# Kernel tuning notes

Hardware: AMD Instinct MI355X
Metric: run time of the kernel (lower is better)

The kernel has to match this reference:

```python
import jax, jax.numpy as jnp
import numpy as np

NEG_SLOPE = 0.2


def _gat_conv(x, edge_index, W, a_src, a_dst, b, heads, out_ch, concat):
    N = x.shape[0]
    # add self loops (PyG GATConv default)
    loops = jnp.arange(N, dtype=edge_index.dtype)
    src = jnp.concatenate([edge_index[0], loops])
    dst = jnp.concatenate([edge_index[1], loops])

    h = (x @ W).reshape(N, heads, out_ch)            # [N,H,C]
    alpha_s = jnp.einsum('nhc,hc->nh', h, a_src)     # [N,H]
    alpha_d = jnp.einsum('nhc,hc->nh', h, a_dst)     # [N,H]
    e = jax.nn.leaky_relu(alpha_s[src] + alpha_d[dst], NEG_SLOPE)  # [E,H]

    # softmax over incoming edges of each dst node (every node has a self loop)
    m = jax.ops.segment_max(e, dst, num_segments=N)  # [N,H]
    e = jnp.exp(e - m[dst])
    denom = jax.ops.segment_sum(e, dst, num_segments=N)  # [N,H]
    alpha = e / denom[dst]                           # [E,H]

    out = jax.ops.segment_sum(h[src] * alpha[..., None], dst, num_segments=N)  # [N,H,C]
    out = out.reshape(N, heads * out_ch) if concat else out.mean(axis=1)
    return out + b


def setup_inputs() -> dict:
    key = jax.random.key(0)
    ks = jax.random.split(key, 12)
    N, E = 100000, 3200000
    F_IN, HID, H1, H2, NCLS = 7, 8, 8, 1, 2
    x = jax.random.normal(ks[0], (N, F_IN), dtype=jnp.float32)
    edge_index = jax.random.randint(ks[1], (2, E), 0, N, dtype=jnp.int64)
    s1 = 1.0 / np.sqrt(F_IN)
    s2 = 1.0 / np.sqrt(HID * H1)
    return {
        'x': x,
        'edge_index': edge_index,
        'W1': jax.random.uniform(ks[2], (F_IN, H1 * HID), jnp.float32, -s1, s1),
        'a_src1': jax.random.uniform(ks[3], (H1, HID), jnp.float32, -s1, s1),
        'a_dst1': jax.random.uniform(ks[4], (H1, HID), jnp.float32, -s1, s1),
        'b1': jnp.zeros((H1 * HID,), jnp.float32),
        'W2': jax.random.uniform(ks[5], (H1 * HID, H2 * NCLS), jnp.float32, -s2, s2),
        'a_src2': jax.random.uniform(ks[6], (H2, NCLS), jnp.float32, -s2, s2),
        'a_dst2': jax.random.uniform(ks[7], (H2, NCLS), jnp.float32, -s2, s2),
        'b2': jnp.zeros((NCLS,), jnp.float32),
    }


def reference(x, edge_index, W1, a_src1, a_dst1, b1, W2, a_src2, a_dst2, b2):
    # eval mode: dropout is identity
    h = _gat_conv(x, edge_index, W1, a_src1, a_dst1, b1, heads=8, out_ch=8, concat=True)
    h = jax.nn.elu(h)
    out = _gat_conv(h, edge_index, W2, a_src2, a_dst2, b2, heads=1, out_ch=2, concat=False)
    return jax.nn.log_softmax(out, axis=1)
```

## Files before the change

kernel.cpp:

```cpp
#include <hip/hip_runtime.h>
#include <math.h>

#define NEG_SLOPE 0.2f
#define L2E 1.4426950408889634f
#define NPB_SHIFT 8
#define NBMAX 512
#define SC_EDGES 16384
#define SC_THREADS 1024
#define CAP 9216

typedef unsigned int u32x4 __attribute__((ext_vector_type(4)));

__device__ __forceinline__ unsigned short f2bf(float f) {
    unsigned int u = __float_as_uint(f);
    u += 0x7FFFu + ((u >> 16) & 1u);
    return (unsigned short)(u >> 16);
}

__global__ void k_h1_scatter(const float* __restrict__ x, const float* __restrict__ W1,
                             const float* __restrict__ a_dst,
                             int N, char* __restrict__ rec,
                             float* __restrict__ ad1,
                             const int* __restrict__ srcA, const int* __restrict__ dstA,
                             int E, int sb, int* __restrict__ cursor_g,
                             unsigned int* __restrict__ payload) {
    __shared__ union {
        struct { int hist[NBMAX]; int gbase[NBMAX]; } sc;
        float ws[7 * 64];
    } smem;
    int t = threadIdx.x;

    if ((int)blockIdx.x < sb) {
        const int ITER = SC_EDGES / SC_THREADS;
        unsigned pay[ITER];
        int meta[ITER];
        int base = blockIdx.x * SC_EDGES;
        int cnt = E - base; if (cnt > SC_EDGES) cnt = SC_EDGES;
        for (int i = t; i < NBMAX; i += SC_THREADS) smem.sc.hist[i] = 0;
        __syncthreads();
#pragma unroll
        for (int k = 0; k < ITER; ++k) {
            int j = k * SC_THREADS + t;
            if (j < cnt) {
                int d = __builtin_nontemporal_load(dstA + base + j);
                int s = __builtin_nontemporal_load(srcA + base + j);
                int b = d >> NPB_SHIFT;
                pay[k] = ((unsigned int)(d & ((1 << NPB_SHIFT) - 1)) << 24) | (unsigned int)s;
                int r = atomicAdd(&smem.sc.hist[b], 1);
                meta[k] = (b << 15) | r;
            } else {
                meta[k] = -1;
            }
        }
        __syncthreads();
        for (int b = t; b < NBMAX; b += SC_THREADS) {
            int c = smem.sc.hist[b];
            smem.sc.gbase[b] = c ? atomicAdd(&cursor_g[b], c) : 0;
        }
        __syncthreads();
#pragma unroll
        for (int k = 0; k < ITER; ++k) {
            if (meta[k] >= 0) {
                int b = meta[k] >> 15;
                int r = meta[k] & 0x7FFF;
                int pos = smem.sc.gbase[b] + r;
                if ((unsigned)pos < CAP)
                    payload[(size_t)b * CAP + pos] = pay[k];
            }
        }
        return;
    }

    for (int i = t; i < 7 * 64; i += SC_THREADS) smem.ws[i] = W1[i];
    __syncthreads();
    int lane = t & 63;
    int base_n = (blockIdx.x - sb) * 64 + (t >> 6) * 4;
    float adv = a_dst[lane];
#pragma unroll
    for (int u = 0; u < 4; ++u) {
        int n = base_n + u;
        if (n >= N) break;
        float hv = 0.f;
#pragma unroll
        for (int k = 0; k < 7; ++k) hv += x[n * 7 + k] * smem.ws[k * 64 + lane];
        ((unsigned short*)(rec + ((size_t)n << 7)))[lane] = f2bf(hv);
        float pd = hv * adv;
#pragma unroll
        for (int off = 1; off < 8; off <<= 1) pd += __shfl_xor(pd, off);
        if ((lane & 7) == 0) ad1[n * 8 + (lane >> 3)] = pd * L2E;
    }
}

__global__ void k_buildcsr(const unsigned int* __restrict__ payload,
                           const int* __restrict__ cursor_g, int N,
                           int2* __restrict__ nrow, int* __restrict__ csr) {
    __shared__ int hist[256], exbase[256], scanb[256];
    const int ITER = (CAP + 1023) / 1024;
    unsigned p[ITER];
    int mt[ITER];
    int b = blockIdx.x;
    int t = threadIdx.x;
    int cntb = cursor_g[b]; if (cntb > CAP) cntb = CAP;
    int bs = b * CAP;
    int nodeBase = b << NPB_SHIFT;
    int nNodes = N - nodeBase; if (nNodes > 256) nNodes = 256;
    if (t < 256) hist[t] = 0;
    __syncthreads();
#pragma unroll
    for (int k = 0; k < ITER; ++k) {
        int i = k * 1024 + t;
        if (i < cntb) {
            p[k] = __builtin_nontemporal_load(payload + bs + i);
            int dl = p[k] >> 24;
            int r = atomicAdd(&hist[dl], 1);
            mt[k] = (dl << 14) | r;
        } else {
            mt[k] = -1;
        }
    }
    __syncthreads();
    if (t < 256) scanb[t] = hist[t];
    __syncthreads();
    for (int off = 1; off < 256; off <<= 1) {
        int u = 0;
        if (t < 256 && t >= off) u = scanb[t - off];
        __syncthreads();
        if (t < 256) scanb[t] += u;
        __syncthreads();
    }
    if (t < 256) {
        int own = hist[t];
        int ex = scanb[t] - own;
        exbase[t] = ex;
        if (t < nNodes) nrow[nodeBase + t] = make_int2(own, bs + ex);
    }
    __syncthreads();
#pragma unroll
    for (int k = 0; k < ITER; ++k) {
        if (mt[k] >= 0) {
            int dl = mt[k] >> 14;
            int r = mt[k] & 0x3FFF;
            csr[bs + exbase[dl] + r] = (int)(p[k] & 0xFFFFFFu);
        }
    }
}

__device__ __forceinline__ void oct_core(
    u32x4 f, float4 awA, float4 awB, float adv, float wm,
    float& den, float& a0, float& a1, float& a2, float& a3,
    float& a4, float& a5, float& a6, float& a7) {
    float f0 = __uint_as_float(f[0] << 16);
    float f1 = __uint_as_float(f[0] & 0xFFFF0000u);
    float f2 = __uint_as_float(f[1] << 16);
    float f3 = __uint_as_float(f[1] & 0xFFFF0000u);
    float f4 = __uint_as_float(f[2] << 16);
    float f5 = __uint_as_float(f[2] & 0xFFFF0000u);
    float f6 = __uint_as_float(f[3] << 16);
    float f7 = __uint_as_float(f[3] & 0xFFFF0000u);
    float p = fmaf(f0, awA.x, adv);
    float q = f1 * awA.y;
    p = fmaf(f2, awA.z, p);
    q = fmaf(f3, awA.w, q);
    p = fmaf(f4, awB.x, p);
    q = fmaf(f5, awB.y, q);
    p = fmaf(f6, awB.z, p);
    q = fmaf(f7, awB.w, q);
    float t = p + q;
    float w = __builtin_amdgcn_exp2f(fmaxf(t, NEG_SLOPE * t)) * wm;
    den += w;
    a0 = fmaf(w, f0, a0);
    a1 = fmaf(w, f1, a1);
    a2 = fmaf(w, f2, a2);
    a3 = fmaf(w, f3, a3);
    a4 = fmaf(w, f4, a4);
    a5 = fmaf(w, f5, a5);
    a6 = fmaf(w, f6, a6);
    a7 = fmaf(w, f7, a7);
}

__global__ void k_agg1(const char* __restrict__ rec, const float* __restrict__ asW,
                       const float* __restrict__ ad1,
                       const int2* __restrict__ nrow,
                       const int* __restrict__ csr, const float* __restrict__ b1,
                       const float* __restrict__ W2, const float* __restrict__ as2w,
                       const float* __restrict__ ad2w, int N,
                       float4* __restrict__ pack) {
    int lane = threadIdx.x & 63;
    int qtr  = lane >> 4;
    int n0 = blockIdx.x * 16 + (threadIdx.x >> 6) * 4 + qtr;
    int n = n0 < N ? n0 : N - 1;
    int ql = lane & 7;
    int s  = (lane >> 3) & 1;
    unsigned foff = (unsigned)(ql << 4);
    float4 awA = ((const float4*)asW)[2 * ql];
    float4 awB = ((const float4*)asW)[2 * ql + 1];
    awA.x *= L2E; awA.y *= L2E; awA.z *= L2E; awA.w *= L2E;
    awB.x *= L2E; awB.y *= L2E; awB.z *= L2E; awB.w *= L2E;
    float adv = ad1[n * 8 + ql];
    int2 dr = nrow[n];
    int d = dr.x;
    int start = dr.y;
    const int* csrb = csr + start;
    int dm1 = d - 1;
    int dmx = max(d, __shfl_xor(d, 16));
    dmx = max(dmx, __shfl_xor(dmx, 32));
    int dmx_s = __builtin_amdgcn_readfirstlane(dmx);
    float a0 = 0.f, a1 = 0.f, a2 = 0.f, a3 = 0.f;
    float a4 = 0.f, a5 = 0.f, a6 = 0.f, a7 = 0.f;
    float den = 0.f;
#define LDR(sv) (*(const u32x4*)(rec + (size_t)((((unsigned)(sv)) << 7) + foff)))
#define QIDX(p) max(min((p), dm1), 0)
    int i1a = csrb[QIDX(s)];
    int i1b = csrb[QIDX(s + 2)];
    int i2a = csrb[QIDX(s + 4)];
    int i2b = csrb[QIDX(s + 6)];
    u32x4 g0a = LDR(i1a);
    u32x4 g0b = LDR(i1b);
    int nst = (dmx_s + 3) >> 2;
#pragma unroll 2
    for (int st = 0; st < nst; ++st) {
        int base4 = st * 4;
        int i3a = csrb[QIDX(base4 + 8 + s)];
        int i3b = csrb[QIDX(base4 + 10 + s)];
        u32x4 g1a = LDR(i2a);
        u32x4 g1b = LDR(i2b);
        float wma = (base4 + s     < d) ? 1.f : 0.f;
        float wmb = (base4 + s + 2 < d) ? 1.f : 0.f;
        oct_core(g0a, awA, awB, adv, wma, den, a0, a1, a2, a3, a4, a5, a6, a7);
        oct_core(g0b, awA, awB, adv, wmb, den, a0, a1, a2, a3, a4, a5, a6, a7);
        g0a = g1a; g0b = g1b;
        i2a = i3a; i2b = i3b;
        (void)i1a; (void)i1b;
    }
    {
        float wm = (s == 0) ? 1.f : 0.f;
        oct_core(LDR(n), awA, awB, adv, wm,
                 den, a0, a1, a2, a3, a4, a5, a6, a7);
    }
#undef QIDX
#undef LDR
    den += __shfl_xor(den, 8);
    a0 += __shfl_xor(a0, 8);
    a1 += __shfl_xor(a1, 8);
    a2 += __shfl_xor(a2, 8);
    a3 += __shfl_xor(a3, 8);
    a4 += __shfl_xor(a4, 8);
    a5 += __shfl_xor(a5, 8);
    a6 += __shfl_xor(a6, 8);
    a7 += __shfl_xor(a7, 8);
    float rden = 1.f / den;
    float4 bbA = ((const float4*)b1)[2 * ql];
    float4 bbB = ((const float4*)b1)[2 * ql + 1];
    float o0 = a0 * rden + bbA.x;
    float o1 = a1 * rden + bbA.y;
    float o2 = a2 * rden + bbA.z;
    float o3 = a3 * rden + bbA.w;
    float o4 = a4 * rden + bbB.x;
    float o5 = a5 * rden + bbB.y;
    float o6 = a6 * rden + bbB.z;
    float o7 = a7 * rden + bbB.w;
    float v0 = o0 > 0.f ? o0 : (__expf(o0) - 1.f);
    float v1 = o1 > 0.f ? o1 : (__expf(o1) - 1.f);
    float v2 = o2 > 0.f ? o2 : (__expf(o2) - 1.f);
    float v3 = o3 > 0.f ? o3 : (__expf(o3) - 1.f);
    float v4 = o4 > 0.f ? o4 : (__expf(o4) - 1.f);
    float v5 = o5 > 0.f ? o5 : (__expf(o5) - 1.f);
    float v6 = o6 > 0.f ? o6 : (__expf(o6) - 1.f);
    float v7 = o7 > 0.f ? o7 : (__expf(o7) - 1.f);
    const float4* W2v = (const float4*)W2;
    float4 w20 = W2v[4 * ql + 0];
    float4 w21 = W2v[4 * ql + 1];
    float4 w22 = W2v[4 * ql + 2];
    float4 w23 = W2v[4 * ql + 3];
    float p0 = v0 * w20.x + v1 * w20.z + v2 * w21.x + v3 * w21.z
             + v4 * w22.x + v5 * w22.z + v6 * w23.x + v7 * w23.z;
    float p1 = v0 * w20.y + v1 * w20.w + v2 * w21.y + v3 * w21.w
             + v4 * w22.y + v5 * w22.w + v6 * w23.y + v7 * w23.w;
#pragma unroll
    for (int off = 1; off < 8; off <<= 1) {
        p0 += __shfl_xor(p0, off);
        p1 += __shfl_xor(p1, off);
    }
    if ((lane & 15) == 0 && n0 < N) {
        float4 pk;
        pk.x = p0;
        pk.y = p1;
        pk.z = (p0 * as2w[0] + p1 * as2w[1]) * L2E;
        pk.w = (p0 * ad2w[0] + p1 * ad2w[1]) * L2E;
        pack[n] = pk;
    }
}

__global__ void k_agg2(const float4* __restrict__ pack, const int2* __restrict__ nrow,
                       const int* __restrict__ csr,
                       const float* __restrict__ b2, int N, float* __restrict__ out) {
    int n = blockIdx.x * 8 + (threadIdx.x >> 5);
    int hl = threadIdx.x & 31;
    if (n >= N) return;
    float4 self = pack[n];
    float adv = self.w;
    int2 dr = nrow[n];
    int d = dr.x;
    int start = dr.y;
    float den = 0.f, a0 = 0.f, a1 = 0.f;
    for (int i = hl; i < d; i += 32) {
        int src = __builtin_nontemporal_load(csr + start + i);
        float4 q = pack[src];
        float t = q.z + adv;
        float w = __builtin_amdgcn_exp2f(fmaxf(t, NEG_SLOPE * t));
        den += w;
        a0 += w * q.x;
        a1 += w * q.y;
    }
#pragma unroll
    for (int off = 1; off < 32; off <<= 1) {
        den += __shfl_xor(den, off);
        a0  += __shfl_xor(a0, off);
        a1  += __shfl_xor(a1, off);
    }
    if (hl == 0) {
        float t = self.z + adv;
        float w = __builtin_amdgcn_exp2f(fmaxf(t, NEG_SLOPE * t));
        den += w;
        a0 += w * self.x;
        a1 += w * self.y;
        float o0 = a0 / den + b2[0];
        float o1 = a1 / den + b2[1];
        float m = fmaxf(o0, o1);
        float lse = m + logf(__expf(o0 - m) + __expf(o1 - m));
        out[n * 2 + 0] = o0 - lse;
        out[n * 2 + 1] = o1 - lse;
    }
}

extern "C" void kernel_launch(void* const* d_in, const int* in_sizes, int n_in,
                              void* d_out, int out_size, void* d_ws, size_t ws_size,
                              hipStream_t stream) {
    const float* x     = (const float*)d_in[0];
    const int*   ei    = (const int*)d_in[1];
    const float* W1    = (const float*)d_in[2];
    const float* as1w  = (const float*)d_in[3];
    const float* ad1w  = (const float*)d_in[4];
    const float* b1    = (const float*)d_in[5];
    const float* W2    = (const float*)d_in[6];
    const float* as2w  = (const float*)d_in[7];
    const float* ad2w  = (const float*)d_in[8];
    const float* b2    = (const float*)d_in[9];
    float* out = (float*)d_out;

    const int N = in_sizes[0] / 7;
    const int E = in_sizes[1] / 2;
    const int* srcA = ei;
    const int* dstA = ei + E;
    const int NB = (N + ((1 << NPB_SHIFT) - 1)) >> NPB_SHIFT;

    size_t off = 0;
    auto alloc = [&](size_t bytes) -> void* {
        void* p = (char*)d_ws + off;
        off += (bytes + 255) & ~(size_t)255;
        return p;
    };
    unsigned int* payload = (unsigned int*)alloc((size_t)NB * CAP * 4);
    char*  rec  = (char*)alloc((size_t)N * 128);
    float* ad1  = (float*)alloc((size_t)N * 8 * 4);
    float4* pack = (float4*)alloc((size_t)N * 16);
    int2*  nrow = (int2*)alloc((size_t)N * 8);
    int*   csr  = (int*)alloc((size_t)NB * CAP * 4);
    int*   cursor_g = (int*)alloc(NBMAX * 4);

    const int nb2 = (N + 63) / 64;
    const int sb  = (E + SC_EDGES - 1) / SC_EDGES;
    const int nb  = (N + 15) / 16;

    hipMemsetAsync(cursor_g, 0, NBMAX * 4, stream);
    k_h1_scatter<<<sb + nb2, SC_THREADS, 0, stream>>>(x, W1, ad1w, N, rec, ad1,
                                                      srcA, dstA, E, sb, cursor_g, payload);
    k_buildcsr<<<NB, 1024, 0, stream>>>(payload, cursor_g, N, nrow, csr);
    k_agg1<<<nb, 256, 0, stream>>>(rec, as1w, ad1, nrow, csr, b1,
                                   W2, as2w, ad2w, N, pack);
    k_agg2<<<(N + 7) / 8, 256, 0, stream>>>(pack, nrow, csr, b2, N, out);
}
```

Measured before the change: 214.7 us.

## Scatter larger edge chunks per block using two-pass histogram and shared cursors

Each scatter block now handles 131072 edges instead of 16384, so far fewer blocks run the scatter phase and far fewer global cursor atomics are issued. Because the per-thread register arrays would no longer fit, the block makes two passes: one to build the per-bucket histogram from dst, and a second that reloads src and dst and takes slots from a shared-memory cursor. This doubles the dst reads and loses the deterministic within-block ordering. It also cuts scatter-phase parallelism to roughly 25 blocks for 3.2M edges, which may leave much of the GPU idle.

After: 406.3 us. +89.3%, slower.

```diff
diff --git a/kernel.cpp b/kernel.cpp
--- a/kernel.cpp
+++ b/kernel.cpp
@@ -5,7 +5,7 @@
 #define L2E 1.4426950408889634f
 #define NPB_SHIFT 8
 #define NBMAX 512
-#define SC_EDGES 16384
+#define SC_EDGES 131072
 #define SC_THREADS 1024
 #define CAP 9216
 
@@ -25,47 +25,41 @@
                              int E, int sb, int* __restrict__ cursor_g,
                              unsigned int* __restrict__ payload) {
     __shared__ union {
-        struct { int hist[NBMAX]; int gbase[NBMAX]; } sc;
+        struct { int hist[NBMAX]; int cur[NBMAX]; } sc;
         float ws[7 * 64];
     } smem;
     int t = threadIdx.x;
 
     if ((int)blockIdx.x < sb) {
-        const int ITER = SC_EDGES / SC_THREADS;
-        unsigned pay[ITER];
-        int meta[ITER];
         int base = blockIdx.x * SC_EDGES;
         int cnt = E - base; if (cnt > SC_EDGES) cnt = SC_EDGES;
         for (int i = t; i < NBMAX; i += SC_THREADS) smem.sc.hist[i] = 0;
         __syncthreads();
-#pragma unroll
-        for (int k = 0; k < ITER; ++k) {
+#pragma unroll 4
+        for (int k = 0; k < SC_EDGES / SC_THREADS; ++k) {
+            int j = k * SC_THREADS + t;
+            if (j < cnt) {
+                int d = dstA[base + j];
+                atomicAdd(&smem.sc.hist[d >> NPB_SHIFT], 1);
+            }
+        }
+        __syncthreads();
+        for (int b = t; b < NBMAX; b += SC_THREADS) {
+            int c = smem.sc.hist[b];
+            smem.sc.cur[b] = c ? atomicAdd(&cursor_g[b], c) : 0;
+        }
+        __syncthreads();
+#pragma unroll 4
+        for (int k = 0; k < SC_EDGES / SC_THREADS; ++k) {
             int j = k * SC_THREADS + t;
             if (j < cnt) {
                 int d = __builtin_nontemporal_load(dstA + base + j);
                 int s = __builtin_nontemporal_load(srcA + base + j);
                 int b = d >> NPB_SHIFT;
-                pay[k] = ((unsigned int)(d & ((1 << NPB_SHIFT) - 1)) << 24) | (unsigned int)s;
-                int r = atomicAdd(&smem.sc.hist[b], 1);
-                meta[k] = (b << 15) | r;
-            } else {
-                meta[k] = -1;
-            }
-        }
-        __syncthreads();
-        for (int b = t; b < NBMAX; b += SC_THREADS) {
-            int c = smem.sc.hist[b];
-            smem.sc.gbase[b] = c ? atomicAdd(&cursor_g[b], c) : 0;
-        }
-        __syncthreads();
-#pragma unroll
-        for (int k = 0; k < ITER; ++k) {
-            if (meta[k] >= 0) {
-                int b = meta[k] >> 15;
-                int r = meta[k] & 0x7FFF;
-                int pos = smem.sc.gbase[b] + r;
+                int pos = atomicAdd(&smem.sc.cur[b], 1);
                 if ((unsigned)pos < CAP)
-                    payload[(size_t)b * CAP + pos] = pay[k];
+                    payload[(size_t)b * CAP + pos] =
+                        ((unsigned int)(d & ((1 << NPB_SHIFT) - 1)) << 24) | (unsigned int)s;
             }
         }
         return;
```

## Fuse CSR build with layer-1 aggregation using shared-memory CSR bucket

Applied to the files above, without the earlier changes.

The separate CSR-building kernel and the first-layer aggregation kernel are merged into one kernel launched per 256-node bucket with 1024 threads. Each block sorts its bucket's edges into a shared-memory CSR (also written to global for layer 2) and then aggregates its 256 nodes in four passes, reading neighbour indices from LDS instead of global memory. This removes one launch and the global CSR round-trip for layer 1. In exchange the grid drops to about 391 large blocks with roughly 37 KB of LDS each, which reduces parallelism and latency hiding for the gather-heavy aggregation.

Result: slower. 224.5 us (+4.6%).

```diff
diff --git a/kernel.cpp b/kernel.cpp
--- a/kernel.cpp
+++ b/kernel.cpp
@@ -88,60 +88,6 @@
 #pragma unroll
         for (int off = 1; off < 8; off <<= 1) pd += __shfl_xor(pd, off);
         if ((lane & 7) == 0) ad1[n * 8 + (lane >> 3)] = pd * L2E;
-    }
-}
-
-__global__ void k_buildcsr(const unsigned int* __restrict__ payload,
-                           const int* __restrict__ cursor_g, int N,
-                           int2* __restrict__ nrow, int* __restrict__ csr) {
-    __shared__ int hist[256], exbase[256], scanb[256];
-    const int ITER = (CAP + 1023) / 1024;
-    unsigned p[ITER];
-    int mt[ITER];
-    int b = blockIdx.x;
-    int t = threadIdx.x;
-    int cntb = cursor_g[b]; if (cntb > CAP) cntb = CAP;
-    int bs = b * CAP;
-    int nodeBase = b << NPB_SHIFT;
-    int nNodes = N - nodeBase; if (nNodes > 256) nNodes = 256;
-    if (t < 256) hist[t] = 0;
-    __syncthreads();
-#pragma unroll
-    for (int k = 0; k < ITER; ++k) {
-        int i = k * 1024 + t;
-        if (i < cntb) {
-            p[k] = __builtin_nontemporal_load(payload + bs + i);
-            int dl = p[k] >> 24;
-            int r = atomicAdd(&hist[dl], 1);
-            mt[k] = (dl << 14) | r;
-        } else {
-            mt[k] = -1;
-        }
-    }
-    __syncthreads();
-    if (t < 256) scanb[t] = hist[t];
-    __syncthreads();
-    for (int off = 1; off < 256; off <<= 1) {
-        int u = 0;
-        if (t < 256 && t >= off) u = scanb[t - off];
-        __syncthreads();
-        if (t < 256) scanb[t] += u;
-        __syncthreads();
-    }
-    if (t < 256) {
-        int own = hist[t];
-        int ex = scanb[t] - own;
-        exbase[t] = ex;
-        if (t < nNodes) nrow[nodeBase + t] = make_int2(own, bs + ex);
-    }
-    __syncthreads();
-#pragma unroll
-    for (int k = 0; k < ITER; ++k) {
-        if (mt[k] >= 0) {
-            int dl = mt[k] >> 14;
-            int r = mt[k] & 0x3FFF;
-            csr[bs + exbase[dl] + r] = (int)(p[k] & 0xFFFFFFu);
-        }
     }
 }
 
@@ -178,17 +124,72 @@
     a7 = fmaf(w, f7, a7);
 }
 
-__global__ void k_agg1(const char* __restrict__ rec, const float* __restrict__ asW,
-                       const float* __restrict__ ad1,
-                       const int2* __restrict__ nrow,
-                       const int* __restrict__ csr, const float* __restrict__ b1,
-                       const float* __restrict__ W2, const float* __restrict__ as2w,
-                       const float* __restrict__ ad2w, int N,
-                       float4* __restrict__ pack) {
-    int lane = threadIdx.x & 63;
+__global__ void k_csragg1(const unsigned int* __restrict__ payload,
+                          const int* __restrict__ cursor_g,
+                          const char* __restrict__ rec, const float* __restrict__ asW,
+                          const float* __restrict__ ad1,
+                          int2* __restrict__ nrow, int* __restrict__ csr,
+                          const float* __restrict__ b1,
+                          const float* __restrict__ W2, const float* __restrict__ as2w,
+                          const float* __restrict__ ad2w, int N,
+                          float4* __restrict__ pack) {
+    __shared__ int hist[256], scanb[256], exbase[256];
+    __shared__ int lcsr[CAP + 8];
+    const int ITER = (CAP + 1023) / 1024;
+    unsigned p[ITER];
+    int mt[ITER];
+    int b = blockIdx.x;
+    int t = threadIdx.x;
+    int cntb = cursor_g[b]; if (cntb > CAP) cntb = CAP;
+    int bs = b * CAP;
+    int nodeBase = b << NPB_SHIFT;
+    int nNodes = N - nodeBase; if (nNodes > 256) nNodes = 256;
+    if (t < 256) hist[t] = 0;
+    __syncthreads();
+#pragma unroll
+    for (int k = 0; k < ITER; ++k) {
+        int i = k * 1024 + t;
+        if (i < cntb) {
+            p[k] = __builtin_nontemporal_load(payload + bs + i);
+            int dl = p[k] >> 24;
+            int r = atomicAdd(&hist[dl], 1);
+            mt[k] = (dl << 14) | r;
+        } else {
+            mt[k] = -1;
+        }
+    }
+    __syncthreads();
+    if (t < 256) scanb[t] = hist[t];
+    __syncthreads();
+    for (int off = 1; off < 256; off <<= 1) {
+        int u = 0;
+        if (t < 256 && t >= off) u = scanb[t - off];
+        __syncthreads();
+        if (t < 256) scanb[t] += u;
+        __syncthreads();
+    }
+    if (t < 256) {
+        int own = hist[t];
+        int ex = scanb[t] - own;
+        exbase[t] = ex;
+        if (t < nNodes) nrow[nodeBase + t] = make_int2(own, bs + ex);
+    }
+    if (t == 0) lcsr[cntb] = 0;
+    __syncthreads();
+#pragma unroll
+    for (int k = 0; k < ITER; ++k) {
+        if (mt[k] >= 0) {
+            int dl = mt[k] >> 14;
+            int r = mt[k] & 0x3FFF;
+            int pos = exbase[dl] + r;
+            int v = (int)(p[k] & 0xFFFFFFu);
+            lcsr[pos] = v;
+            csr[bs + pos] = v;
+        }
+    }
+    __syncthreads();
+    int lane = t & 63;
     int qtr  = lane >> 4;
-    int n0 = blockIdx.x * 16 + (threadIdx.x >> 6) * 4 + qtr;
-    int n = n0 < N ? n0 : N - 1;
     int ql = lane & 7;
     int s  = (lane >> 3) & 1;
     unsigned foff = (unsigned)(ql << 4);
@@ -196,99 +197,102 @@
     float4 awB = ((const float4*)asW)[2 * ql + 1];
     awA.x *= L2E; awA.y *= L2E; awA.z *= L2E; awA.w *= L2E;
     awB.x *= L2E; awB.y *= L2E; awB.z *= L2E; awB.w *= L2E;
-    float adv = ad1[n * 8 + ql];
-    int2 dr = nrow[n];
-    int d = dr.x;
-    int start = dr.y;
-    const int* csrb = csr + start;
-    int dm1 = d - 1;
-    int dmx = max(d, __shfl_xor(d, 16));
-    dmx = max(dmx, __shfl_xor(dmx, 32));
-    int dmx_s = __builtin_amdgcn_readfirstlane(dmx);
-    float a0 = 0.f, a1 = 0.f, a2 = 0.f, a3 = 0.f;
-    float a4 = 0.f, a5 = 0.f, a6 = 0.f, a7 = 0.f;
-    float den = 0.f;
 #define LDR(sv) (*(const u32x4*)(rec + (size_t)((((unsigned)(sv)) << 7) + foff)))
-#define QIDX(p) max(min((p), dm1), 0)
-    int i1a = csrb[QIDX(s)];
-    int i1b = csrb[QIDX(s + 2)];
-    int i2a = csrb[QIDX(s + 4)];
-    int i2b = csrb[QIDX(s + 6)];
-    u32x4 g0a = LDR(i1a);
-    u32x4 g0b = LDR(i1b);
-    int nst = (dmx_s + 3) >> 2;
+#define QIDX(pp) max(min((pp), dm1), 0)
+    for (int pass = 0; pass < 4; ++pass) {
+        int l = pass * 64 + (t >> 6) * 4 + qtr;
+        int n0 = nodeBase + l;
+        int n = n0 < N ? n0 : N - 1;
+        float adv = ad1[n * 8 + ql];
+        int d = hist[l];
+        const int* csrb = lcsr + exbase[l];
+        int dm1 = d - 1;
+        int dmx = max(d, __shfl_xor(d, 16));
+        dmx = max(dmx, __shfl_xor(dmx, 32));
+        int dmx_s = __builtin_amdgcn_readfirstlane(dmx);
+        float a0 = 0.f, a1 = 0.f, a2 = 0.f, a3 = 0.f;
+        float a4 = 0.f, a5 = 0.f, a6 = 0.f, a7 = 0.f;
+        float den = 0.f;
+        int i1a = csrb[QIDX(s)];
+        int i1b = csrb[QIDX(s + 2)];
+        int i2a = csrb[QIDX(s + 4)];
+        int i2b = csrb[QIDX(s + 6)];
+        u32x4 g0a = LDR(i1a);
+        u32x4 g0b = LDR(i1b);
+        int nst = (dmx_s + 3) >> 2;
 #pragma unroll 2
-    for (int st = 0; st < nst; ++st) {
-        int base4 = st * 4;
-        int i3a = csrb[QIDX(base4 + 8 + s)];
-        int i3b = csrb[QIDX(base4 + 10 + s)];
-        u32x4 g1a = LDR(i2a);
-        u32x4 g1b = LDR(i2b);
-        float wma = (base4 + s     < d) ? 1.f : 0.f;
-        float wmb = (base4 + s + 2 < d) ? 1.f : 0.f;
-        oct_core(g0a, awA, awB, adv, wma, den, a0, a1, a2, a3, a4, a5, a6, a7);
-        oct_core(g0b, awA, awB, adv, wmb, den, a0, a1, a2, a3, a4, a5, a6, a7);
-        g0a = g1a; g0b = g1b;
-        i2a = i3a; i2b = i3b;
-        (void)i1a; (void)i1b;
-    }
-    {
-        float wm = (s == 0) ? 1.f : 0.f;
-        oct_core(LDR(n), awA, awB, adv, wm,
-                 den, a0, a1, a2, a3, a4, a5, a6, a7);
+        for (int st = 0; st < nst; ++st) {
+            int base4 = st * 4;
+            int i3a = csrb[QIDX(base4 + 8 + s)];
+            int i3b = csrb[QIDX(base4 + 10 + s)];
+            u32x4 g1a = LDR(i2a);
+            u32x4 g1b = LDR(i2b);
+            float wma = (base4 + s     < d) ? 1.f : 0.f;
+            float wmb = (base4 + s + 2 < d) ? 1.f : 0.f;
+            oct_core(g0a, awA, awB, adv, wma, den, a0, a1, a2, a3, a4, a5, a6, a7);
+            oct_core(g0b, awA, awB, adv, wmb, den, a0, a1, a2, a3, a4, a5, a6, a7);
+            g0a = g1a; g0b = g1b;
+            i2a = i3a; i2b = i3b;
+            (void)i1a; (void)i1b;
+        }
+        {
+            float wm = (s == 0) ? 1.f : 0.f;
+            oct_core(LDR(n), awA, awB, adv, wm,
+                     den, a0, a1, a2, a3, a4, a5, a6, a7);
+        }
+        den += __shfl_xor(den, 8);
+        a0 += __shfl_xor(a0, 8);
+        a1 += __shfl_xor(a1, 8);
+        a2 += __shfl_xor(a2, 8);
+        a3 += __shfl_xor(a3, 8);
+        a4 += __shfl_xor(a4, 8);
+        a5 += __shfl_xor(a5, 8);
+        a6 += __shfl_xor(a6, 8);
+        a7 += __shfl_xor(a7, 8);
+        float rden = 1.f / den;
+        float4 bbA = ((const float4*)b1)[2 * ql];
+        float4 bbB = ((const float4*)b1)[2 * ql + 1];
+        float o0 = a0 * rden + bbA.x;
+        float o1 = a1 * rden + bbA.y;
+        float o2 = a2 * rden + bbA.z;
+        float o3 = a3 * rden + bbA.w;
+        float o4 = a4 * rden + bbB.x;
+        float o5 = a5 * rden + bbB.y;
+        float o6 = a6 * rden + bbB.z;
+        float o7 = a7 * rden + bbB.w;
+        float v0 = o0 > 0.f ? o0 : (__expf(o0) - 1.f);
+        float v1 = o1 > 0.f ? o1 : (__expf(o1) - 1.f);
+        float v2 = o2 > 0.f ? o2 : (__expf(o2) - 1.f);
+        float v3 = o3 > 0.f ? o3 : (__expf(o3) - 1.f);
+        float v4 = o4 > 0.f ? o4 : (__expf(o4) - 1.f);
+        float v5 = o5 > 0.f ? o5 : (__expf(o5) - 1.f);
+        float v6 = o6 > 0.f ? o6 : (__expf(o6) - 1.f);
+        float v7 = o7 > 0.f ? o7 : (__expf(o7) - 1.f);
+        const float4* W2v = (const float4*)W2;
+        float4 w20 = W2v[4 * ql + 0];
+        float4 w21 = W2v[4 * ql + 1];
+        float4 w22 = W2v[4 * ql + 2];
+        float4 w23 = W2v[4 * ql + 3];
+        float p0 = v0 * w20.x + v1 * w20.z + v2 * w21.x + v3 * w21.z
+                 + v4 * w22.x + v5 * w22.z + v6 * w23.x + v7 * w23.z;
+        float p1 = v0 * w20.y + v1 * w20.w + v2 * w21.y + v3 * w21.w
+                 + v4 * w22.y + v5 * w22.w + v6 * w23.y + v7 * w23.w;
+#pragma unroll
+        for (int off = 1; off < 8; off <<= 1) {
+            p0 += __shfl_xor(p0, off);
+            p1 += __shfl_xor(p1, off);
+        }
+        if ((lane & 15) == 0 && n0 < N) {
+            float4 pk;
+            pk.x = p0;
+            pk.y = p1;
+            pk.z = (p0 * as2w[0] + p1 * as2w[1]) * L2E;
+            pk.w = (p0 * ad2w[0] + p1 * ad2w[1]) * L2E;
+            pack[n] = pk;
+        }
     }
 #undef QIDX
 #undef LDR
-    den += __shfl_xor(den, 8);
-    a0 += __shfl_xor(a0, 8);
-    a1 += __shfl_xor(a1, 8);
-    a2 += __shfl_xor(a2, 8);
-    a3 += __shfl_xor(a3, 8);
-    a4 += __shfl_xor(a4, 8);
-    a5 += __shfl_xor(a5, 8);
-    a6 += __shfl_xor(a6, 8);
-    a7 += __shfl_xor(a7, 8);
-    float rden = 1.f / den;
-    float4 bbA = ((const float4*)b1)[2 * ql];
-    float4 bbB = ((const float4*)b1)[2 * ql + 1];
-    float o0 = a0 * rden + bbA.x;
-    float o1 = a1 * rden + bbA.y;
-    float o2 = a2 * rden + bbA.z;
-    float o3 = a3 * rden + bbA.w;
-    float o4 = a4 * rden + bbB.x;
-    float o5 = a5 * rden + bbB.y;
-    float o6 = a6 * rden + bbB.z;
-    float o7 = a7 * rden + bbB.w;
-    float v0 = o0 > 0.f ? o0 : (__expf(o0) - 1.f);
-    float v1 = o1 > 0.f ? o1 : (__expf(o1) - 1.f);
-    float v2 = o2 > 0.f ? o2 : (__expf(o2) - 1.f);
-    float v3 = o3 > 0.f ? o3 : (__expf(o3) - 1.f);
-    float v4 = o4 > 0.f ? o4 : (__expf(o4) - 1.f);
-    float v5 = o5 > 0.f ? o5 : (__expf(o5) - 1.f);
-    float v6 = o6 > 0.f ? o6 : (__expf(o6) - 1.f);
-    float v7 = o7 > 0.f ? o7 : (__expf(o7) - 1.f);
-    const float4* W2v = (const float4*)W2;
-    float4 w20 = W2v[4 * ql + 0];
-    float4 w21 = W2v[4 * ql + 1];
-    float4 w22 = W2v[4 * ql + 2];
-    float4 w23 = W2v[4 * ql + 3];
-    float p0 = v0 * w20.x + v1 * w20.z + v2 * w21.x + v3 * w21.z
-             + v4 * w22.x + v5 * w22.z + v6 * w23.x + v7 * w23.z;
-    float p1 = v0 * w20.y + v1 * w20.w + v2 * w21.y + v3 * w21.w
-             + v4 * w22.y + v5 * w22.w + v6 * w23.y + v7 * w23.w;
-#pragma unroll
-    for (int off = 1; off < 8; off <<= 1) {
-        p0 += __shfl_xor(p0, off);
-        p1 += __shfl_xor(p1, off);
-    }
-    if ((lane & 15) == 0 && n0 < N) {
-        float4 pk;
-        pk.x = p0;
-        pk.y = p1;
-        pk.z = (p0 * as2w[0] + p1 * as2w[1]) * L2E;
-        pk.w = (p0 * ad2w[0] + p1 * ad2w[1]) * L2E;
-        pack[n] = pk;
-    }
 }
 
 __global__ void k_agg2(const float4* __restrict__ pack, const int2* __restrict__ nrow,
@@ -360,7 +364,7 @@
         off += (bytes + 255) & ~(size_t)255;
         return p;
     };
-    unsigned int* payload = (unsigned int*)alloc((size_t)NB * CAP * 4);
+    unsigned int* payload = (unsigned int*)alloc((size_t)NBMAX * CAP * 4);
     char*  rec  = (char*)alloc((size_t)N * 128);
     float* ad1  = (float*)alloc((size_t)N * 8 * 4);
     float4* pack = (float4*)alloc((size_t)N * 16);
@@ -370,13 +374,10 @@
 
     const int nb2 = (N + 63) / 64;
     const int sb  = (E + SC_EDGES - 1) / SC_EDGES;
-    const int nb  = (N + 15) / 16;
-
     hipMemsetAsync(cursor_g, 0, NBMAX * 4, stream);
     k_h1_scatter<<<sb + nb2, SC_THREADS, 0, stream>>>(x, W1, ad1w, N, rec, ad1,
                                                       srcA, dstA, E, sb, cursor_g, payload);
-    k_buildcsr<<<NB, 1024, 0, stream>>>(payload, cursor_g, N, nrow, csr);
-    k_agg1<<<nb, 256, 0, stream>>>(rec, as1w, ad1, nrow, csr, b1,
-                                   W2, as2w, ad2w, N, pack);
+    k_csragg1<<<NB, 1024, 0, stream>>>(payload, cursor_g, rec, as1w, ad1,
+                                       nrow, csr, b1, W2, as2w, ad2w, N, pack);
     k_agg2<<<(N + 7) / 8, 256, 0, stream>>>(pack, nrow, csr, b2, N, out);
 }
```
